# Kernel optimization log

Measured on AMD Instinct MI355X. Metric: run time of the kernel, lower is better.

Reference implementation:

```python
import jax, jax.numpy as jnp
import numpy as np

B, T, N_EMBD = 8, 2048, 512
N_HEAD = 4
EPS = 1e-5
NEG_INF = -1e9


def setup_inputs() -> dict:
    key = jax.random.key(0)
    ks = jax.random.split(key, 10)
    x = jax.random.normal(ks[0], (B, T, N_EMBD), dtype=jnp.float32)
    # relative-position index map [t, t] into a (2t-1)-entry boolean mask table
    pos_emb = jax.random.randint(ks[1], (T, T), 0, 2 * T - 1)
    ln_w = jax.random.normal(ks[2], (N_EMBD,), dtype=jnp.float32) * 0.02 + 1.0
    ln_b = jax.random.normal(ks[3], (N_EMBD,), dtype=jnp.float32) * 0.02
    aff_w = jax.random.normal(ks[4], (N_EMBD,), dtype=jnp.float32) * 0.02 + 1.0
    aff_b = jax.random.normal(ks[5], (N_EMBD,), dtype=jnp.float32) * 0.02
    W_qkv = jax.random.normal(ks[6], (N_EMBD, 3 * N_EMBD), dtype=jnp.float32) * (N_EMBD ** -0.5)
    # boolean lookup table; True = position visible (mostly visible)
    mask_table = jax.random.uniform(ks[7], (2 * T - 1,)) > 0.2
    W_proj = jax.random.normal(ks[8], (N_EMBD, N_EMBD), dtype=jnp.float32) * (N_EMBD ** -0.5)
    return {
        "x": x, "pos_emb": pos_emb, "ln_w": ln_w, "ln_b": ln_b,
        "aff_w": aff_w, "aff_b": aff_b, "W_qkv": W_qkv,
        "mask_table": mask_table, "W_proj": W_proj,
    }


def reference(x, pos_emb, ln_w, ln_b, aff_w, aff_b, W_qkv, mask_table, W_proj):
    b, t, n = x.shape
    hd = n // N_HEAD
    # LayerNorm (mean subtract, rms normalize, affine)
    x = x - jnp.mean(x, axis=-1, keepdims=True)
    x = x * jax.lax.rsqrt(jnp.mean(x * x, axis=-1, keepdims=True) + EPS)
    x = x * ln_w + ln_b
    # extra affine (onnx initializers 7/8) then fused QKV projection
    x = x * aff_w + aff_b
    qkv = x @ W_qkv                       # [b, t, 3n]
    q, k, v = jnp.split(qkv, 3, axis=2)
    q = q.reshape(b, t, N_HEAD, hd).transpose(0, 2, 1, 3)  # [b, h, t, hd]
    k = k.reshape(b, t, N_HEAD, hd).transpose(0, 2, 1, 3)
    v = v.reshape(b, t, N_HEAD, hd).transpose(0, 2, 1, 3)
    scale = 1.0 / np.sqrt(hd).astype(np.float32)
    scores = jnp.einsum('bhqd,bhkd->bhqk', q, k) * scale   # [b, h, t, t]
    # gather-based relative-position mask: True = attend, False = mask out
    mask = mask_table[pos_emb]                             # [t, t] bool
    scores = jnp.where(mask, scores, NEG_INF)
    attn = jax.nn.softmax(scores, axis=-1)
    out = jnp.einsum('bhqk,bhkd->bhqd', attn, v)           # [b, h, t, hd]
    out = out.transpose(0, 2, 1, 3).reshape(b, t, n)
    return out @ W_proj
```

## Files before the change

kernel.cpp:

```cpp
#include <hip/hip_runtime.h>
#include <hip/hip_bf16.h>

#define T_SEQ 2048
#define NEMBD 512
#define NHEAD 4
#define HDIM  128
#define BATCH 8
#define MROWS (BATCH * T_SEQ)
#define QSCALE 0.12751744534f

typedef __attribute__((ext_vector_type(8))) short short8;
typedef __attribute__((ext_vector_type(4))) short short4v;
typedef __attribute__((ext_vector_type(4))) float f32x4;

static __device__ __forceinline__ float bf2f(unsigned short h) {
  return __uint_as_float(((unsigned int)h) << 16);
}
static __device__ __forceinline__ short f2bs(float f) {
  unsigned int u = __float_as_uint(f);
  unsigned int r = (u + 0x7FFFu + ((u >> 16) & 1u)) >> 16;
  return (short)r;
}
static __device__ __forceinline__ unsigned int pk2(float a, float b) {
  __hip_bfloat162 h = __float22bfloat162_rn(make_float2(a, b));
  return *reinterpret_cast<unsigned int*>(&h);
}
static __device__ __forceinline__ int mask_at(const void* mt, int fmt, int idx) {
  if (fmt == 0) return ((const int*)mt)[idx] != 0;
  if (fmt == 1) return ((const unsigned char*)mt)[idx] != 0;
  if (fmt == 2) return ((const float*)mt)[idx] != 0.0f;
  return ((const unsigned short*)mt)[idx] != 0;
}
static __device__ __forceinline__ int pos_at(const int* pos, int i64, size_t idx) {
  return i64 ? pos[idx * 2] : pos[idx];
}
static __device__ __forceinline__ void gload16(const void* g, void* l) {
  __builtin_amdgcn_global_load_lds((const __attribute__((address_space(1))) void*)g,
                                   (__attribute__((address_space(3))) void*)l,
                                   16, 0, 0);
}

__global__ __launch_bounds__(256) void detect_kernel(
    const unsigned int* __restrict__ mt, const unsigned int* __restrict__ posw,
    int* __restrict__ flags)
{
  __shared__ int s01, sf, sbf, szero;
  const int t = threadIdx.x;
  if (t == 0) { s01 = 1; sf = 1; sbf = 1; szero = 0; }
  __syncthreads();
  int a01 = 1, af = 1, ab = 1, zc = 0;
  for (int i = t; i < 1023; i += 256) {
    const unsigned int v = mt[i];
    if (v > 1u) a01 = 0;
    const float f = __uint_as_float(v);
    if (!(f == 0.0f || f == 1.0f)) af = 0;
    const unsigned int lo = v & 0xFFFFu, hi = v >> 16;
    if (!((lo == 0u || lo == 0x3F80u) && (hi == 0u || hi == 0x3F80u))) ab = 0;
  }
  for (int i = t; i < 512; i += 256) if (posw[2 * i + 1] == 0u) zc++;
  if (!a01) atomicAnd(&s01, 0);
  if (!af)  atomicAnd(&sf, 0);
  if (!ab)  atomicAnd(&sbf, 0);
  if (zc)   atomicAdd(&szero, zc);
  __syncthreads();
  if (t == 0) {
    flags[0] = s01 ? 0 : (sf ? 2 : (sbf ? 3 : 1));
    flags[2] = (szero > 500) ? 1 : 0;
  }
}

__global__ __launch_bounds__(256) void pack_mask_kernel(
    const int* __restrict__ pos, const void* __restrict__ mt,
    const int* __restrict__ flags, unsigned int* __restrict__ mp)
{
  const int idx = blockIdx.x * 256 + threadIdx.x;
  const int fmt = flags[0];
  const int i64 = flags[2];
  const int q = idx >> 6;
  const int wrd = idx & 63;
  const size_t base = (size_t)q * T_SEQ + wrd * 32;
  unsigned int bits = 0;
  #pragma unroll 4
  for (int j = 0; j < 32; ++j)
    bits |= (mask_at(mt, fmt, pos_at(pos, i64, base + j)) ? 1u : 0u) << j;
  mp[idx] = bits;
}

__global__ __launch_bounds__(256) void vecprep_kernel(
    const float* __restrict__ lnw, const float* __restrict__ lnb,
    const float* __restrict__ afw, const float* __restrict__ afb,
    float* __restrict__ effw, float* __restrict__ effb)
{
  const int c = blockIdx.x * 256 + threadIdx.x;
  if (c >= NEMBD) return;
  effw[c] = lnw[c] * afw[c];
  effb[c] = lnb[c] * afw[c] + afb[c];
}

__global__ __launch_bounds__(256) void wconv2t_kernel(
    const float* __restrict__ Wq, const float* __restrict__ Wp,
    short* __restrict__ WqT, short* __restrict__ WpT)
{
  __shared__ float lds[64][65];
  int bid = blockIdx.x;
  const float* W; short* Wt; int N, n0, k0;
  if (bid < 192) { W = Wq; Wt = WqT; N = 1536; n0 = (bid % 24) * 64; k0 = (bid / 24) * 64; }
  else { bid -= 192; W = Wp; Wt = WpT; N = 512; n0 = (bid & 7) * 64; k0 = (bid >> 3) * 64; }
  const int tc = threadIdx.x & 63, tr = threadIdx.x >> 6;
  #pragma unroll
  for (int i = 0; i < 16; ++i) {
    const int kl = tr * 16 + i;
    lds[kl][tc] = W[(size_t)(k0 + kl) * N + n0 + tc];
  }
  __syncthreads();
  #pragma unroll
  for (int i = 0; i < 16; ++i) {
    const int nl = tr * 16 + i;
    Wt[(size_t)(n0 + nl) * 512 + k0 + tc] = f2bs(lds[tc][nl]);
  }
}

__global__ __launch_bounds__(64) void ln_kernel(
    const float* __restrict__ x, const float* __restrict__ effw, const float* __restrict__ effb,
    short* __restrict__ xp)
{
  const int row = blockIdx.x;
  const int tid = threadIdx.x;
  const float4* p = (const float4*)(x + (size_t)row * NEMBD + tid * 8);
  const float4 a0 = p[0], a1 = p[1];
  float f[8] = {a0.x, a0.y, a0.z, a0.w, a1.x, a1.y, a1.z, a1.w};
  float s = 0.f, s2 = 0.f;
  #pragma unroll
  for (int j = 0; j < 8; ++j) { s += f[j]; s2 += f[j] * f[j]; }
  #pragma unroll
  for (int off = 1; off < 64; off <<= 1) {
    s  += __shfl_xor(s, off);
    s2 += __shfl_xor(s2, off);
  }
  const float mean = s * (1.0f / NEMBD);
  const float rstd = rsqrtf(s2 * (1.0f / NEMBD) - mean * mean + 1e-5f);
  const float4* wp = (const float4*)(effw + tid * 8);
  const float4* bp = (const float4*)(effb + tid * 8);
  const float4 w0 = wp[0], w1 = wp[1], b0 = bp[0], b1 = bp[1];
  short8 ob;
  ob[0] = f2bs((f[0] - mean) * rstd * w0.x + b0.x);
  ob[1] = f2bs((f[1] - mean) * rstd * w0.y + b0.y);
  ob[2] = f2bs((f[2] - mean) * rstd * w0.z + b0.z);
  ob[3] = f2bs((f[3] - mean) * rstd * w0.w + b0.w);
  ob[4] = f2bs((f[4] - mean) * rstd * w1.x + b1.x);
  ob[5] = f2bs((f[5] - mean) * rstd * w1.y + b1.y);
  ob[6] = f2bs((f[6] - mean) * rstd * w1.z + b1.z);
  ob[7] = f2bs((f[7] - mean) * rstd * w1.w + b1.w);
  *((short8*)(xp + (size_t)row * NEMBD + tid * 8)) = ob;
}

template<int MODE>
__global__ __launch_bounds__(256) void gemm_kernel(
    const short* __restrict__ A, const short* __restrict__ Bt,
    void* __restrict__ out0, short* __restrict__ Kp, short* __restrict__ Vt)
{
  __shared__ alignas(16) short Atile[128 * 64];
  __shared__ alignas(16) short Btile[128 * 64];
  const int tid = threadIdx.x;
  const int l = tid & 63;
  const int w = tid >> 6;
  const int m0 = blockIdx.x * 128;
  const int n0 = blockIdx.y * 128;
  const int w_r = w >> 1, w_c = w & 1;
  const int lr = l & 15, lg = l >> 4;
  const int key = lr & 7;
  f32x4 acc[4][4] = {};

  for (int kt = 0; kt < 512; kt += 64) {
    #pragma unroll
    for (int i = 0; i < 4; ++i) {
      const int c = i * 256 + tid;
      const int row = c >> 3, col8 = c & 7;
      gload16(A  + (size_t)(m0 + row) * 512 + kt + (col8 ^ (row & 7)) * 8,
              Atile + (i * 256 + w * 64) * 8);
      gload16(Bt + (size_t)(n0 + row) * 512 + kt + (col8 ^ (row & 7)) * 8,
              Btile + (i * 256 + w * 64) * 8);
    }
    __syncthreads();
    #pragma unroll
    for (int kk = 0; kk < 2; ++kk) {
      short8 af[4], bfm[4];
      #pragma unroll
      for (int m = 0; m < 4; ++m)
        af[m] = *(const short8*)((char*)Atile
            + (w_r * 64 + m * 16 + lr) * 128 + ((kk * 4 + lg) ^ key) * 16);
      #pragma unroll
      for (int n = 0; n < 4; ++n)
        bfm[n] = *(const short8*)((char*)Btile
            + (w_c * 64 + n * 16 + lr) * 128 + ((kk * 4 + lg) ^ key) * 16);
      #pragma unroll
      for (int m = 0; m < 4; ++m)
        #pragma unroll
        for (int n = 0; n < 4; ++n)
          acc[m][n] = __builtin_amdgcn_mfma_f32_16x16x32_bf16(af[m], bfm[n], acc[m][n], 0, 0, 0);
    }
    __syncthreads();
  }

  if (MODE == 1) {
    float* out = (float*)out0;
    #pragma unroll
    for (int m = 0; m < 4; ++m)
      #pragma unroll
      for (int n = 0; n < 4; ++n)
        #pragma unroll
        for (int r = 0; r < 4; ++r) {
          const int gm = m0 + w_r * 64 + m * 16 + lg * 4 + r;
          const int gn = n0 + w_c * 64 + n * 16 + lr;
          out[(size_t)gm * NEMBD + gn] = acc[m][n][r];
        }
  } else {
    const int which = n0 >> 9;
    const int h = (n0 >> 7) & 3;
    short* Qp = (short*)out0;
    #pragma unroll
    for (int m = 0; m < 4; ++m)
      #pragma unroll
      for (int n = 0; n < 4; ++n)
        #pragma unroll
        for (int r = 0; r < 4; ++r) {
          const int gm = m0 + w_r * 64 + m * 16 + lg * 4 + r;
          const int b = gm >> 11, t = gm & 2047;
          const int d = w_c * 64 + n * 16 + lr;
          const size_t bh = (size_t)((b << 2) | h);
          const float v = acc[m][n][r];
          if (which == 0)      Qp[(bh * T_SEQ + t) * HDIM + d] = f2bs(v * QSCALE);
          else if (which == 1) Kp[(bh * T_SEQ + t) * HDIM + d] = f2bs(v);
          else                 Vt[(bh * HDIM + d) * T_SEQ + t] = f2bs(v);
        }
  }
}

__global__ __launch_bounds__(512, 4) void attn_kernel(
    const short* __restrict__ Q, const short* __restrict__ Kp, const short* __restrict__ Vt,
    const unsigned int* __restrict__ maskP, short* __restrict__ O)
{
  __shared__ alignas(16) short Kt[3][32 * 128];
  __shared__ alignas(16) short Vs[3][128 * 32];
  __shared__ alignas(16) short Pw[8][16 * 40];
  const int tid = threadIdx.x;
  const int l = tid & 63;
  const int w = tid >> 6;
  const int lr = l & 15, lg = l >> 4;
  const int s7 = lr & 7;
  const int vkey = (lr >> 1) & 3;
  const int swz = ((blockIdx.x & 7) << 6) | (blockIdx.x >> 3);
  const int bh = swz >> 4;
  const int q0 = (swz & 15) * 128 + w * 16;
  const short* Qb = Q  + (size_t)bh * T_SEQ * HDIM;
  const short* Kb = Kp + (size_t)bh * T_SEQ * HDIM;
  const short* Vb = Vt + (size_t)bh * HDIM * T_SEQ;

  const int kr = tid >> 4, kc = tid & 15;
  const int vr = tid >> 2, vc = tid & 3;
  #define STAGE(b, kti) do {                                                        \
    const int kt_ = (kti) * 32;                                                     \
    gload16(Kb + (size_t)(kt_ + kr) * HDIM + (kc ^ (kr & 7)) * 8,                   \
            (char*)&Kt[b][0] + w * 1024);                                           \
    gload16(Vb + (size_t)vr * T_SEQ + kt_ + (vc ^ ((vr >> 1) & 3)) * 8,             \
            (char*)&Vs[b][0] + w * 1024);                                           \
  } while (0)

  short8 aq[4];
  #pragma unroll
  for (int kk = 0; kk < 4; ++kk)
    aq[kk] = *(const short8*)(Qb + (size_t)(q0 + lr) * HDIM + kk * 32 + lg * 8);

  float lsum = 0.f;
  f32x4 acc[8] = {};
  const size_t mrow = (size_t)(q0 + lr) * 64;

  STAGE(0, 0);
  int bc = 0, bn = 1;
  for (int kti = 0; kti < 64; ++kti) {
    if (kti + 1 < 64) {
      STAGE(bn, kti + 1);
      asm volatile("s_waitcnt vmcnt(2)" ::: "memory");
    } else {
      asm volatile("s_waitcnt vmcnt(0)" ::: "memory");
    }
    __builtin_amdgcn_sched_barrier(0);
    __builtin_amdgcn_s_barrier();
    const unsigned int mq = maskP[mrow + kti];
    f32x4 sn[2];
    __builtin_amdgcn_s_setprio(1);
    #pragma unroll
    for (int n = 0; n < 2; ++n) {
      f32x4 s = {};
      #pragma unroll
      for (int kk = 0; kk < 4; ++kk) {
        const short8 bk = *(const short8*)((char*)&Kt[bc][0]
            + (n * 16 + lr) * 256 + ((kk * 4 + lg) ^ s7) * 16);
        s = __builtin_amdgcn_mfma_f32_16x16x32_bf16(bk, aq[kk], s, 0, 0, 0);
      }
      sn[n] = s;
    }
    __builtin_amdgcn_s_setprio(0);
    #pragma unroll
    for (int n = 0; n < 2; ++n) {
      const int base = n * 16 + lg * 4;
      const float p0 = __builtin_amdgcn_exp2f(((mq >> (base + 0)) & 1) ? sn[n][0] : -1e9f);
      const float p1 = __builtin_amdgcn_exp2f(((mq >> (base + 1)) & 1) ? sn[n][1] : -1e9f);
      const float p2 = __builtin_amdgcn_exp2f(((mq >> (base + 2)) & 1) ? sn[n][2] : -1e9f);
      const float p3 = __builtin_amdgcn_exp2f(((mq >> (base + 3)) & 1) ? sn[n][3] : -1e9f);
      lsum += (p0 + p1) + (p2 + p3);
      union { short4v s4; unsigned int u[2]; } pwv;
      pwv.u[0] = pk2(p0, p1);
      pwv.u[1] = pk2(p2, p3);
      *(short4v*)&Pw[w][lr * 40 + base] = pwv.s4;
    }
    const short8 pa = *(const short8*)&Pw[w][lr * 40 + lg * 8];
    __builtin_amdgcn_s_setprio(1);
    #pragma unroll
    for (int nn = 0; nn < 8; ++nn) {
      const short8 bv = *(const short8*)((char*)&Vs[bc][0]
          + (nn * 16 + lr) * 64 + (lg ^ vkey) * 16);
      acc[nn] = __builtin_amdgcn_mfma_f32_16x16x32_bf16(pa, bv, acc[nn], 0, 0, 0);
    }
    __builtin_amdgcn_s_setprio(0);
    bc = bn;
    bn = (bn == 2) ? 0 : bn + 1;
  }
  #undef STAGE

  float s = lsum;
  s += __shfl_xor(s, 16);
  s += __shfl_xor(s, 32);
  const float rin = 1.0f / s;
  float rin4[4];
  #pragma unroll
  for (int r = 0; r < 4; ++r) rin4[r] = __shfl(rin, lg * 4 + r);
  const int b = bh >> 2, h = bh & 3;
  #pragma unroll
  for (int nn = 0; nn < 8; ++nn) {
    const int d = nn * 16 + lr;
    #pragma unroll
    for (int r = 0; r < 4; ++r) {
      const int qg = q0 + lg * 4 + r;
      O[((size_t)b * T_SEQ + qg) * NEMBD + h * HDIM + d] = f2bs(acc[nn][r] * rin4[r]);
    }
  }
}

__global__ __launch_bounds__(256) void fill_kernel(float* __restrict__ out, float v, size_t n) {
  for (size_t i = blockIdx.x * 256 + threadIdx.x; i < n; i += (size_t)gridDim.x * 256)
    out[i] = v;
}

extern "C" void kernel_launch(void* const* d_in, const int* in_sizes, int n_in,
                              void* d_out, int out_size, void* d_ws, size_t ws_size,
                              hipStream_t stream)
{
  const float* x     = (const float*)d_in[0];
  const int*   pos   = (const int*)d_in[1];
  const float* lnw   = (const float*)d_in[2];
  const float* lnb   = (const float*)d_in[3];
  const float* afw   = (const float*)d_in[4];
  const float* afb   = (const float*)d_in[5];
  const float* Wqkv  = (const float*)d_in[6];
  const void*  mtab  = d_in[7];
  const float* Wproj = (const float*)d_in[8];

  size_t off = 0;
  char* ws = (char*)d_ws;
  int* flags = (int*)(ws + off);                   off += 256;
  float* effw = (float*)(ws + off);                off += 2048;
  float* effb = (float*)(ws + off);                off += 2048;
  unsigned int* maskP = (unsigned int*)(ws + off); off += (size_t)T_SEQ * 64 * 4;
  short* Xp  = (short*)(ws + off);                 off += (size_t)MROWS * NEMBD * 2;
  short* WqT = (short*)(ws + off);                 off += (size_t)3 * NEMBD * NEMBD * 2;
  short* WpT = (short*)(ws + off);                 off += (size_t)NEMBD * NEMBD * 2;
  short* Qb  = (short*)(ws + off);                 off += (size_t)BATCH * NHEAD * T_SEQ * HDIM * 2;
  short* Kb  = (short*)(ws + off);                 off += (size_t)BATCH * NHEAD * T_SEQ * HDIM * 2;
  short* Vt  = (short*)(ws + off);                 off += (size_t)BATCH * NHEAD * T_SEQ * HDIM * 2;
  short* Ob  = Xp;

  if (ws_size < off) {
    fill_kernel<<<256, 256, 0, stream>>>((float*)d_out, (float)(ws_size >> 20), (size_t)out_size);
    return;
  }

  detect_kernel<<<1, 256, 0, stream>>>((const unsigned int*)mtab, (const unsigned int*)pos, flags);
  pack_mask_kernel<<<(T_SEQ * (T_SEQ / 32)) / 256, 256, 0, stream>>>(pos, mtab, flags, maskP);
  vecprep_kernel<<<2, 256, 0, stream>>>(lnw, lnb, afw, afb, effw, effb);
  wconv2t_kernel<<<256, 256, 0, stream>>>(Wqkv, Wproj, WqT, WpT);
  ln_kernel<<<MROWS, 64, 0, stream>>>(x, effw, effb, Xp);
  dim3 g0(128, 12);
  gemm_kernel<0><<<g0, 256, 0, stream>>>(Xp, WqT, (void*)Qb, Kb, Vt);
  attn_kernel<<<512, 512, 0, stream>>>(Qb, Kb, Vt, maskP, Ob);
  dim3 g1(128, 4);
  gemm_kernel<1><<<g1, 256, 0, stream>>>(Ob, WpT, d_out, nullptr, nullptr);
}
```

Before: 210.0 us.

## Fold detect and vecprep into other kernels; build P operand in registers

The format-detection kernel is merged into the mask packing kernel, with every block recomputing the flags in shared memory. The effective LN weight/bias prep runs as an extra block of the weight transpose kernel. Together these remove two launches. In attention, the per-wave LDS round trip for the probability tile is dropped: P is packed straight into the MFMA A operand in registers, and the V operand is read as two 8-byte halves with a matching permuted k ordering. This saves LDS writes and reads per tile but doubles the number of V loads and adds redundant detection work in every packing block.

```diff
diff --git a/kernel.cpp b/kernel.cpp
--- a/kernel.cpp
+++ b/kernel.cpp
@@ -40,42 +40,36 @@
                                    16, 0, 0);
 }
 
-__global__ __launch_bounds__(256) void detect_kernel(
-    const unsigned int* __restrict__ mt, const unsigned int* __restrict__ posw,
-    int* __restrict__ flags)
+__global__ __launch_bounds__(256) void pack_mask_kernel(
+    const int* __restrict__ pos, const void* __restrict__ mt,
+    unsigned int* __restrict__ mp)
 {
   __shared__ int s01, sf, sbf, szero;
   const int t = threadIdx.x;
   if (t == 0) { s01 = 1; sf = 1; sbf = 1; szero = 0; }
   __syncthreads();
-  int a01 = 1, af = 1, ab = 1, zc = 0;
-  for (int i = t; i < 1023; i += 256) {
-    const unsigned int v = mt[i];
-    if (v > 1u) a01 = 0;
-    const float f = __uint_as_float(v);
-    if (!(f == 0.0f || f == 1.0f)) af = 0;
-    const unsigned int lo = v & 0xFFFFu, hi = v >> 16;
-    if (!((lo == 0u || lo == 0x3F80u) && (hi == 0u || hi == 0x3F80u))) ab = 0;
-  }
-  for (int i = t; i < 512; i += 256) if (posw[2 * i + 1] == 0u) zc++;
-  if (!a01) atomicAnd(&s01, 0);
-  if (!af)  atomicAnd(&sf, 0);
-  if (!ab)  atomicAnd(&sbf, 0);
-  if (zc)   atomicAdd(&szero, zc);
-  __syncthreads();
-  if (t == 0) {
-    flags[0] = s01 ? 0 : (sf ? 2 : (sbf ? 3 : 1));
-    flags[2] = (szero > 500) ? 1 : 0;
-  }
-}
-
-__global__ __launch_bounds__(256) void pack_mask_kernel(
-    const int* __restrict__ pos, const void* __restrict__ mt,
-    const int* __restrict__ flags, unsigned int* __restrict__ mp)
-{
+  {
+    const unsigned int* mtw = (const unsigned int*)mt;
+    const unsigned int* posw = (const unsigned int*)pos;
+    int a01 = 1, af = 1, ab = 1, zc = 0;
+    for (int i = t; i < 1023; i += 256) {
+      const unsigned int v = mtw[i];
+      if (v > 1u) a01 = 0;
+      const float f = __uint_as_float(v);
+      if (!(f == 0.0f || f == 1.0f)) af = 0;
+      const unsigned int lo = v & 0xFFFFu, hi = v >> 16;
+      if (!((lo == 0u || lo == 0x3F80u) && (hi == 0u || hi == 0x3F80u))) ab = 0;
+    }
+    for (int i = t; i < 512; i += 256) if (posw[2 * i + 1] == 0u) zc++;
+    if (!a01) atomicAnd(&s01, 0);
+    if (!af)  atomicAnd(&sf, 0);
+    if (!ab)  atomicAnd(&sbf, 0);
+    if (zc)   atomicAdd(&szero, zc);
+    __syncthreads();
+  }
+  const int fmt = s01 ? 0 : (sf ? 2 : (sbf ? 3 : 1));
+  const int i64 = (szero > 500) ? 1 : 0;
   const int idx = blockIdx.x * 256 + threadIdx.x;
-  const int fmt = flags[0];
-  const int i64 = flags[2];
   const int q = idx >> 6;
   const int wrd = idx & 63;
   const size_t base = (size_t)q * T_SEQ + wrd * 32;
@@ -86,23 +80,24 @@
   mp[idx] = bits;
 }
 
-__global__ __launch_bounds__(256) void vecprep_kernel(
+__global__ __launch_bounds__(256) void wconv2t_kernel(
+    const float* __restrict__ Wq, const float* __restrict__ Wp,
+    short* __restrict__ WqT, short* __restrict__ WpT,
     const float* __restrict__ lnw, const float* __restrict__ lnb,
     const float* __restrict__ afw, const float* __restrict__ afb,
     float* __restrict__ effw, float* __restrict__ effb)
 {
-  const int c = blockIdx.x * 256 + threadIdx.x;
-  if (c >= NEMBD) return;
-  effw[c] = lnw[c] * afw[c];
-  effb[c] = lnb[c] * afw[c] + afb[c];
-}
-
-__global__ __launch_bounds__(256) void wconv2t_kernel(
-    const float* __restrict__ Wq, const float* __restrict__ Wp,
-    short* __restrict__ WqT, short* __restrict__ WpT)
-{
+  int bid = blockIdx.x;
+  if (bid == 256) {
+    #pragma unroll
+    for (int i = 0; i < 2; ++i) {
+      const int c = i * 256 + threadIdx.x;
+      effw[c] = lnw[c] * afw[c];
+      effb[c] = lnb[c] * afw[c] + afb[c];
+    }
+    return;
+  }
   __shared__ float lds[64][65];
-  int bid = blockIdx.x;
   const float* W; short* Wt; int N, n0, k0;
   if (bid < 192) { W = Wq; Wt = WqT; N = 1536; n0 = (bid % 24) * 64; k0 = (bid / 24) * 64; }
   else { bid -= 192; W = Wp; Wt = WpT; N = 512; n0 = (bid & 7) * 64; k0 = (bid >> 3) * 64; }
@@ -242,7 +237,6 @@
 {
   __shared__ alignas(16) short Kt[3][32 * 128];
   __shared__ alignas(16) short Vs[3][128 * 32];
-  __shared__ alignas(16) short Pw[8][16 * 40];
   const int tid = threadIdx.x;
   const int l = tid & 63;
   const int w = tid >> 6;
@@ -274,6 +268,9 @@
   float lsum = 0.f;
   f32x4 acc[8] = {};
   const size_t mrow = (size_t)(q0 + lr) * 64;
+  const int c0 = ((lg >> 1) + 0) ^ vkey;
+  const int c1 = ((lg >> 1) + 2) ^ vkey;
+  const int hb = (lg & 1) * 8;
 
   STAGE(0, 0);
   int bc = 0, bn = 1;
@@ -301,6 +298,7 @@
       sn[n] = s;
     }
     __builtin_amdgcn_s_setprio(0);
+    union { short8 s8; unsigned int u[4]; } pau;
     #pragma unroll
     for (int n = 0; n < 2; ++n) {
       const int base = n * 16 + lg * 4;
@@ -309,18 +307,18 @@
       const float p2 = __builtin_amdgcn_exp2f(((mq >> (base + 2)) & 1) ? sn[n][2] : -1e9f);
       const float p3 = __builtin_amdgcn_exp2f(((mq >> (base + 3)) & 1) ? sn[n][3] : -1e9f);
       lsum += (p0 + p1) + (p2 + p3);
-      union { short4v s4; unsigned int u[2]; } pwv;
-      pwv.u[0] = pk2(p0, p1);
-      pwv.u[1] = pk2(p2, p3);
-      *(short4v*)&Pw[w][lr * 40 + base] = pwv.s4;
-    }
-    const short8 pa = *(const short8*)&Pw[w][lr * 40 + lg * 8];
+      pau.u[n * 2 + 0] = pk2(p0, p1);
+      pau.u[n * 2 + 1] = pk2(p2, p3);
+    }
+    const char* vbase = (const char*)&Vs[bc][0];
     __builtin_amdgcn_s_setprio(1);
     #pragma unroll
     for (int nn = 0; nn < 8; ++nn) {
-      const short8 bv = *(const short8*)((char*)&Vs[bc][0]
-          + (nn * 16 + lr) * 64 + (lg ^ vkey) * 16);
-      acc[nn] = __builtin_amdgcn_mfma_f32_16x16x32_bf16(pa, bv, acc[nn], 0, 0, 0);
+      const int rowb = (nn * 16 + lr) * 64;
+      union { short8 s8; short4v h[2]; } bvu;
+      bvu.h[0] = *(const short4v*)(vbase + rowb + c0 * 16 + hb);
+      bvu.h[1] = *(const short4v*)(vbase + rowb + c1 * 16 + hb);
+      acc[nn] = __builtin_amdgcn_mfma_f32_16x16x32_bf16(pau.s8, bvu.s8, acc[nn], 0, 0, 0);
     }
     __builtin_amdgcn_s_setprio(0);
     bc = bn;
@@ -368,7 +366,6 @@
 
   size_t off = 0;
   char* ws = (char*)d_ws;
-  int* flags = (int*)(ws + off);                   off += 256;
   float* effw = (float*)(ws + off);                off += 2048;
   float* effb = (float*)(ws + off);                off += 2048;
   unsigned int* maskP = (unsigned int*)(ws + off); off += (size_t)T_SEQ * 64 * 4;
@@ -385,10 +382,8 @@
     return;
   }
 
-  detect_kernel<<<1, 256, 0, stream>>>((const unsigned int*)mtab, (const unsigned int*)pos, flags);
-  pack_mask_kernel<<<(T_SEQ * (T_SEQ / 32)) / 256, 256, 0, stream>>>(pos, mtab, flags, maskP);
-  vecprep_kernel<<<2, 256, 0, stream>>>(lnw, lnb, afw, afb, effw, effb);
-  wconv2t_kernel<<<256, 256, 0, stream>>>(Wqkv, Wproj, WqT, WpT);
+  pack_mask_kernel<<<(T_SEQ * (T_SEQ / 32)) / 256, 256, 0, stream>>>(pos, mtab, maskP);
+  wconv2t_kernel<<<257, 256, 0, stream>>>(Wqkv, Wproj, WqT, WpT, lnw, lnb, afw, afb, effw, effb);
   ln_kernel<<<MROWS, 64, 0, stream>>>(x, effw, effb, Xp);
   dim3 g0(128, 12);
   gemm_kernel<0><<<g0, 256, 0, stream>>>(Xp, WqT, (void*)Qb, Kb, Vt);
```

Result: slower. 225.9 us (+7.6%).
